# Optimization experiments

Measured on AMD Instinct MI355X. Metric: run time of the kernel, lower is better.

Reference implementation:

```python
import jax, jax.numpy as jnp
import numpy as np

INPUT_SIZE = 4
SEQ = 256
EMB = 64
QKV = 64
BATCH = 64
INDICES = np.array([0, 0, 1, 1])
BLK = SEQ // INPUT_SIZE                      # 64 positions per block
POS_GROUP = np.repeat(INDICES, BLK)          # per-position group id, shape [SEQ]
NUM_HEADS = len(np.unique(INDICES))          # 2
GROUP_POS = [np.where(POS_GROUP == g)[0] for g in range(NUM_HEADS)]  # static index sets


def _linear_params(key, din, dout):
    # torch nn.Linear default init: U(-1/sqrt(din), 1/sqrt(din))
    kw, kb = jax.random.split(key)
    s = 1.0 / np.sqrt(din)
    W = jax.random.uniform(kw, (dout, din), jnp.float32, -s, s)
    b = jax.random.uniform(kb, (dout,), jnp.float32, -s, s)
    return W, b


def setup_inputs() -> dict:
    key = jax.random.key(0)
    keys = jax.random.split(key, 1 + 3 * NUM_HEADS)
    inp = {"x": jax.random.normal(keys[0], (BATCH, SEQ, EMB), jnp.float32)}
    for g in range(NUM_HEADS):
        L = len(GROUP_POS[g])                # 128
        din, dout = L * EMB, L * QKV         # 8192 -> 8192
        WQ, bQ = _linear_params(keys[1 + 3 * g + 0], din, dout)
        WK, bK = _linear_params(keys[1 + 3 * g + 1], din, dout)
        WV, bV = _linear_params(keys[1 + 3 * g + 2], din, dout)
        inp[f"WQ{g}"], inp[f"bQ{g}"] = WQ, bQ
        inp[f"WK{g}"], inp[f"bK{g}"] = WK, bK
        inp[f"WV{g}"], inp[f"bV{g}"] = WV, bV
    return inp


def _head(xs, WQ, bQ, WK, bK, WV, bV, L):
    # xs: [B, L*EMB] flattened group slice
    B = xs.shape[0]
    Q = (xs @ WQ.T + bQ).reshape(B, L, QKV)
    K = (xs @ WK.T + bK).reshape(B, L, QKV)
    V = (xs @ WV.T + bV).reshape(B, L, QKV)
    scores = jnp.einsum("bik,bjk->bij", Q, K)        # [B, L, L]
    # Original uses nn.Softmax(dim=1): normalize over the QUERY axis (axis=1).
    attn = jax.nn.softmax(scores, axis=1)
    Z = jnp.einsum("bij,bjk->bik", attn, V)
    # coeff applied AFTER attention @ V, as in the original
    return Z * (1.0 / jnp.sqrt(jnp.float32(QKV)))


def reference(x, WQ0, bQ0, WK0, bK0, WV0, bV0, WQ1, bQ1, WK1, bK1, WV1, bV1):
    params = [(WQ0, bQ0, WK0, bK0, WV0, bV0), (WQ1, bQ1, WK1, bK1, WV1, bV1)]
    B = x.shape[0]
    out = jnp.zeros((B, SEQ, QKV), jnp.float32)
    for g in range(NUM_HEADS):                        # small static loop over groups
        pos = GROUP_POS[g]
        L = len(pos)
        xs = x[:, pos, :].reshape(B, L * EMB)
        Z = _head(xs, *params[g], L)
        out = out.at[:, pos, :].set(Z)
    return out
```

## Files before the change

### kernel.cpp

```cpp
#include <hip/hip_runtime.h>
#include <hip/hip_bf16.h>

#define BATCH 64
#define SEQ   256
#define EMB   64
#define QKVD  64
#define KD    8192
#define ND    8192
#define SEQD  16384
#define BK    64
#define NCHUNK (KD / BK)

typedef __attribute__((ext_vector_type(8))) short bf16x8;
typedef __attribute__((ext_vector_type(4))) float f32x4;

struct WArgs { const float* W[6]; const float* b[6]; };

__device__ __forceinline__ short f2bf(float f) {
    unsigned u = __builtin_bit_cast(unsigned, f);
    u += 0x7fffu + ((u >> 16) & 1u);
    return (short)(u >> 16);
}

__device__ __forceinline__ void gl16(const void* g, void* l) {
    __builtin_amdgcn_global_load_lds(
        (const __attribute__((address_space(1))) void*)g,
        (__attribute__((address_space(3))) void*)l, 16, 0, 0);
}

__global__ __launch_bounds__(256)
void cvt_x_kernel(const float* __restrict__ x, short* __restrict__ xb) {
    const int i = (blockIdx.x * 256 + threadIdx.x) * 4;
    float4 v = *reinterpret_cast<const float4*>(x + i);
    short4 o;
    o.x = f2bf(v.x); o.y = f2bf(v.y); o.z = f2bf(v.z); o.w = f2bf(v.w);
    *reinterpret_cast<short4*>(xb + i) = o;
}

__global__ __launch_bounds__(256, 3)
void qkv_gemm_kernel(const short* __restrict__ xb, WArgs wa,
                     float* __restrict__ qkv) {
    __shared__ __attribute__((aligned(16))) short A_lds[2][64 * 64];
    __shared__ __attribute__((aligned(16))) float W_lds[2][64 * 64];

    const int gi = blockIdx.y;
    const int g  = gi / 3;
    const int wv = threadIdx.x >> 6;
    const int ln = threadIdx.x & 63;
    const int r  = ln & 15;
    const int kb = ln >> 4;
    const int n0 = blockIdx.x * 64;

    const float* __restrict__ Wg = wa.W[gi];

    const int a_m = ln >> 3;
    const int a_c = (ln & 7) ^ (ln >> 3);
    const int w_r = ln >> 4;

    f32x4 acc0 = {0.f, 0.f, 0.f, 0.f};
    f32x4 acc1 = acc0, acc2 = acc0, acc3 = acc0;

    auto stage = [&](int t, int buf) {
        const short* As = xb + g * KD + t * BK;
        #pragma unroll
        for (int ii = 0; ii < 2; ++ii) {
            const int i = wv * 2 + ii;
            const short* src = As + (size_t)(i * 8 + a_m) * SEQD + a_c * 8;
            gl16(src, (char*)&A_lds[buf][0] + i * 1024);
        }
        const float* Ws = Wg + (size_t)n0 * KD + t * BK;
        #pragma unroll
        for (int jj = 0; jj < 4; ++jj) {
            const int j = wv * 4 + jj;
            const int nrow = j * 4 + w_r;
            const int c = (ln & 15) ^ (nrow & 7);
            const float* src = Ws + (size_t)nrow * KD + c * 4;
            gl16(src, (char*)&W_lds[buf][0] + j * 1024);
        }
    };

    auto compute = [&](int buf) {
        const short* Ab = &A_lds[buf][0];
        const float* Wb = &W_lds[buf][0];
        const int wrow = wv * 16 + r;
        #pragma unroll
        for (int kk = 0; kk < 2; ++kk) {
            const int c0 = kk * 8 + kb * 2;
            f32x4 w0 = *(const f32x4*)(Wb + wrow * 64 + ((c0       ^ (r & 7)) * 4));
            f32x4 w1 = *(const f32x4*)(Wb + wrow * 64 + (((c0 + 1) ^ (r & 7)) * 4));
            bf16x8 bb;
            bb[0] = f2bf(w0[0]); bb[1] = f2bf(w0[1]); bb[2] = f2bf(w0[2]); bb[3] = f2bf(w0[3]);
            bb[4] = f2bf(w1[0]); bb[5] = f2bf(w1[1]); bb[6] = f2bf(w1[2]); bb[7] = f2bf(w1[3]);
            const int ac = ((kk * 4 + kb) ^ (r & 7)) * 8;
            const bf16x8 a0 = *(const bf16x8*)(Ab + (0 * 16 + r) * 64 + ac);
            const bf16x8 a1 = *(const bf16x8*)(Ab + (1 * 16 + r) * 64 + ac);
            const bf16x8 a2 = *(const bf16x8*)(Ab + (2 * 16 + r) * 64 + ac);
            const bf16x8 a3 = *(const bf16x8*)(Ab + (3 * 16 + r) * 64 + ac);
            acc0 = __builtin_amdgcn_mfma_f32_16x16x32_bf16(a0, bb, acc0, 0, 0, 0);
            acc1 = __builtin_amdgcn_mfma_f32_16x16x32_bf16(a1, bb, acc1, 0, 0, 0);
            acc2 = __builtin_amdgcn_mfma_f32_16x16x32_bf16(a2, bb, acc2, 0, 0, 0);
            acc3 = __builtin_amdgcn_mfma_f32_16x16x32_bf16(a3, bb, acc3, 0, 0, 0);
        }
    };

    stage(0, 0);
    __syncthreads();
    for (int t = 0; t < NCHUNK - 1; ++t) {
        stage(t + 1, (t + 1) & 1);
        compute(t & 1);
        __syncthreads();
    }
    compute((NCHUNK - 1) & 1);

    const int nbr = n0 + wv * 16 + r;
    const float bias = wa.b[gi][nbr];
    float* orow = qkv + (size_t)gi * (BATCH * ND) + nbr;
    #pragma unroll
    for (int reg = 0; reg < 4; ++reg) {
        const int m = kb * 4 + reg;
        orow[(size_t)(m)      * ND] = acc0[reg] + bias;
        orow[(size_t)(m + 16) * ND] = acc1[reg] + bias;
        orow[(size_t)(m + 32) * ND] = acc2[reg] + bias;
        orow[(size_t)(m + 48) * ND] = acc3[reg] + bias;
    }
}

__global__ __launch_bounds__(256)
void attn_kernel(const float* __restrict__ qkv, float* __restrict__ out) {
    __shared__ float Ql[128 * 65];
    __shared__ float Kl[128 * 65];
    __shared__ float Sc[128 * 129];
    __shared__ float Pm[256];
    __shared__ float Ps[256];
    __shared__ float Rden[128];

    const int b = blockIdx.x;
    const int g = blockIdx.y;
    const int t = threadIdx.x;

    const float* __restrict__ Qg = qkv + ((size_t)(3 * g + 0) * BATCH + b) * ND;
    const float* __restrict__ Kg = qkv + ((size_t)(3 * g + 1) * BATCH + b) * ND;
    const float* __restrict__ Vg = qkv + ((size_t)(3 * g + 2) * BATCH + b) * ND;

    for (int e = t; e < 8192; e += 256) {
        const int i = e >> 6, k = e & 63;
        Ql[i * 65 + k] = Qg[e];
        Kl[i * 65 + k] = Kg[e];
    }
    __syncthreads();

    {
        const int i0 = (t >> 4) * 8;
        const int j0 = (t & 15) * 8;
        float s[8][8];
        #pragma unroll
        for (int rr = 0; rr < 8; ++rr)
            #pragma unroll
            for (int cc = 0; cc < 8; ++cc) s[rr][cc] = 0.f;
        for (int k = 0; k < 64; ++k) {
            float qv[8], kv[8];
            #pragma unroll
            for (int rr = 0; rr < 8; ++rr) qv[rr] = Ql[(i0 + rr) * 65 + k];
            #pragma unroll
            for (int cc = 0; cc < 8; ++cc) kv[cc] = Kl[(j0 + cc) * 65 + k];
            #pragma unroll
            for (int rr = 0; rr < 8; ++rr)
                #pragma unroll
                for (int cc = 0; cc < 8; ++cc)
                    s[rr][cc] = fmaf(qv[rr], kv[cc], s[rr][cc]);
        }
        #pragma unroll
        for (int rr = 0; rr < 8; ++rr)
            #pragma unroll
            for (int cc = 0; cc < 8; ++cc)
                Sc[(i0 + rr) * 129 + (j0 + cc)] = s[rr][cc];
    }
    __syncthreads();

    const int j = t & 127, h = t >> 7;
    {
        for (int e = t; e < 8192; e += 256) {
            const int i = e >> 6, k = e & 63;
            Ql[i * 65 + k] = Vg[e];
        }
        float m = -3.0e38f;
        for (int i = h * 64; i < h * 64 + 64; ++i)
            m = fmaxf(m, Sc[i * 129 + j]);
        Pm[h * 128 + j] = m;
    }
    __syncthreads();
    {
        const float m = fmaxf(Pm[j], Pm[128 + j]);
        float sum = 0.f;
        for (int i = h * 64; i < h * 64 + 64; ++i) {
            const float e = __expf(Sc[i * 129 + j] - m);
            Sc[i * 129 + j] = e;
            sum += e;
        }
        Ps[h * 128 + j] = sum;
    }
    __syncthreads();
    if (t < 128) Rden[t] = 1.0f / (Ps[t] + Ps[128 + t]);
    __syncthreads();

    {
        const int i0 = (t >> 4) * 8;
        const int k0 = (t & 15) * 4;
        float z[8][4];
        #pragma unroll
        for (int rr = 0; rr < 8; ++rr)
            #pragma unroll
            for (int cc = 0; cc < 4; ++cc) z[rr][cc] = 0.f;
        for (int jj = 0; jj < 128; ++jj) {
            const float rd = Rden[jj];
            float av[8], vv[4];
            #pragma unroll
            for (int rr = 0; rr < 8; ++rr) av[rr] = Sc[(i0 + rr) * 129 + jj] * rd;
            #pragma unroll
            for (int cc = 0; cc < 4; ++cc) vv[cc] = Ql[jj * 65 + k0 + cc];
            #pragma unroll
            for (int rr = 0; rr < 8; ++rr)
                #pragma unroll
                for (int cc = 0; cc < 4; ++cc)
                    z[rr][cc] = fmaf(av[rr], vv[cc], z[rr][cc]);
        }
        float* op = out + (size_t)b * (SEQ * QKVD) + (size_t)(g * 128) * QKVD + k0;
        #pragma unroll
        for (int rr = 0; rr < 8; ++rr) {
            float4 o;
            o.x = z[rr][0] * 0.125f; o.y = z[rr][1] * 0.125f;
            o.z = z[rr][2] * 0.125f; o.w = z[rr][3] * 0.125f;
            *reinterpret_cast<float4*>(op + (size_t)(i0 + rr) * QKVD) = o;
        }
    }
}

extern "C" void kernel_launch(void* const* d_in, const int* in_sizes, int n_in,
                              void* d_out, int out_size, void* d_ws, size_t ws_size,
                              hipStream_t stream) {
    const float* x = (const float*)d_in[0];
    WArgs wa;
    for (int g = 0; g < 2; ++g)
        for (int q = 0; q < 3; ++q) {
            wa.W[g * 3 + q] = (const float*)d_in[1 + g * 6 + q * 2];
            wa.b[g * 3 + q] = (const float*)d_in[2 + g * 6 + q * 2];
        }

    short* xb  = (short*)d_ws;
    float* qkv = (float*)((char*)d_ws + (size_t)4 * 1024 * 1024);

    cvt_x_kernel<<<dim3(1024), dim3(256), 0, stream>>>(x, xb);
    qkv_gemm_kernel<<<dim3(ND / 64, 6), dim3(256), 0, stream>>>(xb, wa, qkv);
    attn_kernel<<<dim3(BATCH, 2), dim3(256), 0, stream>>>(qkv, (float*)d_out);
}
```

Measured before the change: 358.7 us.

## Restructure QKV GEMM as persistent per-wave W streaming with register-held A

```diff
diff --git a/kernel.cpp b/kernel.cpp
--- a/kernel.cpp
+++ b/kernel.cpp
@@ -8,8 +8,8 @@
 #define KD    8192
 #define ND    8192
 #define SEQD  16384
-#define BK    64
-#define NCHUNK (KD / BK)
+#define BKT   256
+#define NTK   (KD / BKT)
 
 typedef __attribute__((ext_vector_type(8))) short bf16x8;
 typedef __attribute__((ext_vector_type(4))) float f32x4;
@@ -37,91 +37,95 @@
     *reinterpret_cast<short4*>(xb + i) = o;
 }
 
-__global__ __launch_bounds__(256, 3)
+__global__ __launch_bounds__(256, 1)
 void qkv_gemm_kernel(const short* __restrict__ xb, WArgs wa,
                      float* __restrict__ qkv) {
-    __shared__ __attribute__((aligned(16))) short A_lds[2][64 * 64];
-    __shared__ __attribute__((aligned(16))) float W_lds[2][64 * 64];
-
-    const int gi = blockIdx.y;
-    const int g  = gi / 3;
+    __shared__ __attribute__((aligned(16))) float W_lds[4][2][16 * BKT];
+
     const int wv = threadIdx.x >> 6;
     const int ln = threadIdx.x & 63;
     const int r  = ln & 15;
     const int kb = ln >> 4;
-    const int n0 = blockIdx.x * 64;
-
-    const float* __restrict__ Wg = wa.W[gi];
-
-    const int a_m = ln >> 3;
-    const int a_c = (ln & 7) ^ (ln >> 3);
-    const int w_r = ln >> 4;
-
-    f32x4 acc0 = {0.f, 0.f, 0.f, 0.f};
-    f32x4 acc1 = acc0, acc2 = acc0, acc3 = acc0;
-
-    auto stage = [&](int t, int buf) {
-        const short* As = xb + g * KD + t * BK;
-        #pragma unroll
-        for (int ii = 0; ii < 2; ++ii) {
-            const int i = wv * 2 + ii;
-            const short* src = As + (size_t)(i * 8 + a_m) * SEQD + a_c * 8;
-            gl16(src, (char*)&A_lds[buf][0] + i * 1024);
-        }
-        const float* Ws = Wg + (size_t)n0 * KD + t * BK;
-        #pragma unroll
-        for (int jj = 0; jj < 4; ++jj) {
-            const int j = wv * 4 + jj;
-            const int nrow = j * 4 + w_r;
-            const int c = (ln & 15) ^ (nrow & 7);
-            const float* src = Ws + (size_t)nrow * KD + c * 4;
-            gl16(src, (char*)&W_lds[buf][0] + j * 1024);
-        }
-    };
-
-    auto compute = [&](int buf) {
-        const short* Ab = &A_lds[buf][0];
-        const float* Wb = &W_lds[buf][0];
-        const int wrow = wv * 16 + r;
-        #pragma unroll
-        for (int kk = 0; kk < 2; ++kk) {
-            const int c0 = kk * 8 + kb * 2;
-            f32x4 w0 = *(const f32x4*)(Wb + wrow * 64 + ((c0       ^ (r & 7)) * 4));
-            f32x4 w1 = *(const f32x4*)(Wb + wrow * 64 + (((c0 + 1) ^ (r & 7)) * 4));
-            bf16x8 bb;
-            bb[0] = f2bf(w0[0]); bb[1] = f2bf(w0[1]); bb[2] = f2bf(w0[2]); bb[3] = f2bf(w0[3]);
-            bb[4] = f2bf(w1[0]); bb[5] = f2bf(w1[1]); bb[6] = f2bf(w1[2]); bb[7] = f2bf(w1[3]);
-            const int ac = ((kk * 4 + kb) ^ (r & 7)) * 8;
-            const bf16x8 a0 = *(const bf16x8*)(Ab + (0 * 16 + r) * 64 + ac);
-            const bf16x8 a1 = *(const bf16x8*)(Ab + (1 * 16 + r) * 64 + ac);
-            const bf16x8 a2 = *(const bf16x8*)(Ab + (2 * 16 + r) * 64 + ac);
-            const bf16x8 a3 = *(const bf16x8*)(Ab + (3 * 16 + r) * 64 + ac);
-            acc0 = __builtin_amdgcn_mfma_f32_16x16x32_bf16(a0, bb, acc0, 0, 0, 0);
-            acc1 = __builtin_amdgcn_mfma_f32_16x16x32_bf16(a1, bb, acc1, 0, 0, 0);
-            acc2 = __builtin_amdgcn_mfma_f32_16x16x32_bf16(a2, bb, acc2, 0, 0, 0);
-            acc3 = __builtin_amdgcn_mfma_f32_16x16x32_bf16(a3, bb, acc3, 0, 0, 0);
-        }
-    };
-
-    stage(0, 0);
-    __syncthreads();
-    for (int t = 0; t < NCHUNK - 1; ++t) {
-        stage(t + 1, (t + 1) & 1);
-        compute(t & 1);
-        __syncthreads();
-    }
-    compute((NCHUNK - 1) & 1);
-
-    const int nbr = n0 + wv * 16 + r;
-    const float bias = wa.b[gi][nbr];
-    float* orow = qkv + (size_t)gi * (BATCH * ND) + nbr;
-    #pragma unroll
-    for (int reg = 0; reg < 4; ++reg) {
-        const int m = kb * 4 + reg;
-        orow[(size_t)(m)      * ND] = acc0[reg] + bias;
-        orow[(size_t)(m + 16) * ND] = acc1[reg] + bias;
-        orow[(size_t)(m + 32) * ND] = acc2[reg] + bias;
-        orow[(size_t)(m + 48) * ND] = acc3[reg] + bias;
+
+    float* const Wl0 = &W_lds[wv][0][0];
+    float* const Wl1 = &W_lds[wv][1][0];
+
+    for (int nt = 0; nt < 3; ++nt) {
+        const int logical = blockIdx.x * 3 + nt;
+        const int gi = logical >> 7;
+        const int n0 = (logical & 127) * 64;
+        const int g  = gi / 3;
+
+        const char*  __restrict__ Wbase =
+            (const char*)(wa.W[gi] + (size_t)(n0 + wv * 16) * KD);
+        const short* __restrict__ Ag = xb + g * KD;
+
+        f32x4 acc0 = {0.f, 0.f, 0.f, 0.f};
+        f32x4 acc1 = acc0, acc2 = acc0, acc3 = acc0;
+
+        auto stage = [&](int t, float* slot) {
+            const char* tb = Wbase + (size_t)t * (BKT * 4);
+            #pragma unroll
+            for (int row = 0; row < 16; ++row) {
+                gl16(tb + (size_t)row * (KD * 4) + ((ln ^ (row & 7)) << 4),
+                     (char*)slot + row * 1024);
+            }
+        };
+
+        stage(0, Wl0);
+        stage(1, Wl1);
+
+        for (int t = 0; t < NTK; ++t) {
+            float* slot = (t & 1) ? Wl1 : Wl0;
+
+            bf16x8 afr[32];
+            {
+                const short* Ab = Ag + t * BKT + kb * 8;
+                #pragma unroll
+                for (int s = 0; s < 8; ++s)
+                    #pragma unroll
+                    for (int mi = 0; mi < 4; ++mi)
+                        afr[s * 4 + mi] = *(const bf16x8*)
+                            (Ab + (size_t)(mi * 16 + r) * SEQD + s * 32);
+            }
+
+            asm volatile("s_waitcnt vmcnt(0)" ::: "memory");
+            __builtin_amdgcn_sched_barrier(0);
+
+            const float* wrow = slot + r * BKT;
+            const int key = r & 7;
+            #pragma unroll
+            for (int s = 0; s < 8; ++s) {
+                const int c0 = s * 8 + kb * 2;
+                f32x4 w0 = *(const f32x4*)(wrow + (((c0)     ^ key) * 4));
+                f32x4 w1 = *(const f32x4*)(wrow + (((c0 + 1) ^ key) * 4));
+                bf16x8 bb;
+                bb[0] = f2bf(w0[0]); bb[1] = f2bf(w0[1]);
+                bb[2] = f2bf(w0[2]); bb[3] = f2bf(w0[3]);
+                bb[4] = f2bf(w1[0]); bb[5] = f2bf(w1[1]);
+                bb[6] = f2bf(w1[2]); bb[7] = f2bf(w1[3]);
+                acc0 = __builtin_amdgcn_mfma_f32_16x16x32_bf16(afr[s*4+0], bb, acc0, 0, 0, 0);
+                acc1 = __builtin_amdgcn_mfma_f32_16x16x32_bf16(afr[s*4+1], bb, acc1, 0, 0, 0);
+                acc2 = __builtin_amdgcn_mfma_f32_16x16x32_bf16(afr[s*4+2], bb, acc2, 0, 0, 0);
+                acc3 = __builtin_amdgcn_mfma_f32_16x16x32_bf16(afr[s*4+3], bb, acc3, 0, 0, 0);
+            }
+
+            asm volatile("s_waitcnt lgkmcnt(0)" ::: "memory");
+            __builtin_amdgcn_sched_barrier(0);
+            if (t + 2 < NTK) stage(t + 2, slot);
+        }
+
+        const int nbr = n0 + wv * 16 + r;
+        const float bias = wa.b[gi][nbr];
+        float* orow = qkv + (size_t)gi * (BATCH * ND) + nbr;
+        #pragma unroll
+        for (int reg = 0; reg < 4; ++reg) {
+            const int m = kb * 4 + reg;
+            orow[(size_t)(m)      * ND] = acc0[reg] + bias;
+            orow[(size_t)(m + 16) * ND] = acc1[reg] + bias;
+            orow[(size_t)(m + 32) * ND] = acc2[reg] + bias;
+            orow[(size_t)(m + 48) * ND] = acc3[reg] + bias;
+        }
     }
 }
 
@@ -250,6 +254,6 @@
     float* qkv = (float*)((char*)d_ws + (size_t)4 * 1024 * 1024);
 
     cvt_x_kernel<<<dim3(1024), dim3(256), 0, stream>>>(x, xb);
-    qkv_gemm_kernel<<<dim3(ND / 64, 6), dim3(256), 0, stream>>>(xb, wa, qkv);
+    qkv_gemm_kernel<<<dim3(256), dim3(256), 0, stream>>>(xb, wa, qkv);
     attn_kernel<<<dim3(BATCH, 2), dim3(256), 0, stream>>>(qkv, (float*)d_out);
 }
```

New measurement: 483.2 us. 34.7% more time.
